# Performance work log

Hardware: AMD Instinct MI355X
Metric: run time of the kernel (lower is better)

The kernel has to match this reference:

```python
import jax, jax.numpy as jnp
import numpy as np

B, D, T, H, E = 4, 1024, 2048, 16, 64  # batch, dim, seq_len, n_heads, hidden_dim (H*E == D)


def setup_inputs() -> dict:
    key = jax.random.key(0)
    ks = jax.random.split(key, 6)
    x = jax.random.normal(ks[0], (B, D, T), dtype=jnp.float32)            # (b, e, t) layout
    Wp = jax.random.normal(ks[1], (H, E, D), dtype=jnp.float32) / np.sqrt(D)  # per-head proj weights
    bp = jax.random.normal(ks[2], (H, E), dtype=jnp.float32) * 0.01
    tw = jax.random.normal(ks[3], (H, T), dtype=jnp.float32) / np.sqrt(T)  # per-head Toeplitz kernel, tw[h,0]=diagonal
    Wo = jax.random.normal(ks[4], (D, D), dtype=jnp.float32) / np.sqrt(D)
    bo = jax.random.normal(ks[5], (D,), dtype=jnp.float32) * 0.01
    return {"x": x, "Wp": Wp, "bp": bp, "tw": tw, "Wo": Wo, "bo": bo}


def reference(x, Wp, bp, tw, Wo, bo):
    # x: (b, dim, t) -> (b, t, dim)
    xt = jnp.transpose(x, (0, 2, 1))
    # per-head projections: (b, h, e, t)
    proj = jnp.einsum('btd,hed->bhet', xt, Wp) + bp[None, :, :, None]
    # build per-head causal lower-triangular Toeplitz matrices: Tm[h, t, s] = tw[h, t-s] if s <= t else 0
    idx = jnp.arange(T)[:, None] - jnp.arange(T)[None, :]  # (t, s)
    Tm = jnp.where(idx >= 0, tw[:, jnp.clip(idx, 0)], 0.0)  # (h, t, s)
    # causal Toeplitz mixing along time per head
    mixed = jnp.einsum('hts,bhes->bhet', Tm, proj)          # (b, h, e, t)
    # concat heads on feature dim: (b, t, h*e) == (b, t, dim)
    cat = jnp.transpose(mixed, (0, 3, 1, 2)).reshape(B, T, H * E)
    out = cat @ Wo.T + bo                                   # out_proj: Linear(dim, dim)
    return jnp.transpose(out, (0, 2, 1))                    # back to (b, e, t)
```

## Files before the change

kernel.cpp:

```cpp
#include <hip/hip_runtime.h>
#include <cstdint>

#define NB 4
#define ND 1024
#define NT 2048
#define NH 16
#define NE 64
#define GLEN 2240
#define CAP 2312

typedef __bf16 bf16x8 __attribute__((ext_vector_type(8)));
typedef float f32x4 __attribute__((ext_vector_type(4)));
typedef unsigned short us8 __attribute__((ext_vector_type(8)));
typedef unsigned short us4 __attribute__((ext_vector_type(4)));

__device__ __forceinline__ unsigned short f2bf(float f) {
  unsigned u = __builtin_bit_cast(unsigned, f);
  return (unsigned short)((u + 0x7fffu + ((u >> 16) & 1u)) >> 16);
}

__device__ __forceinline__ void gload16(const void* g, void* l) {
  __builtin_amdgcn_global_load_lds(
      (const __attribute__((address_space(1))) void*)(uintptr_t)g,
      (__attribute__((address_space(3))) void*)(uintptr_t)l, 16, 0, 0);
}

__global__ __launch_bounds__(256) void prep_transpose(const float* __restrict__ x,
                                                      unsigned short* __restrict__ xT,
                                                      const float* __restrict__ Wp,
                                                      const float* __restrict__ Wo,
                                                      const float* __restrict__ tw,
                                                      unsigned short* __restrict__ WpB,
                                                      unsigned short* __restrict__ WoB,
                                                      unsigned short* __restrict__ Gr8) {
  __shared__ float tile[64][65];
  if (blockIdx.x >= 32) {
    int bid = (blockIdx.x - 32) + 8 * (blockIdx.y + 16 * blockIdx.z);
    int idx = bid * 256 + threadIdx.x;
    const int stride = 512 * 256;
    const int n4 = ND * ND / 4;
    for (int i = idx; i < n4; i += stride) {
      float4 v = ((const float4*)Wp)[i];
      us4 o = {f2bf(v.x), f2bf(v.y), f2bf(v.z), f2bf(v.w)};
      ((us4*)WpB)[i] = o;
    }
    for (int i = idx; i < n4; i += stride) {
      float4 v = ((const float4*)Wo)[i];
      us4 o = {f2bf(v.x), f2bf(v.y), f2bf(v.z), f2bf(v.w)};
      ((us4*)WoB)[i] = o;
    }
    for (int i = idx; i < NH * 8 * GLEN; i += stride) {
      int h = i / (8 * GLEN);
      int rem = i - h * 8 * GLEN;
      int r = rem / GLEN;
      int c = rem - r * GLEN;
      int src = c + r;
      Gr8[i] = (src <= NT - 1) ? f2bf(tw[h * NT + (NT - 1) - src]) : (unsigned short)0;
    }
    return;
  }
  const int c = threadIdx.x & 15, r = threadIdx.x >> 4;
  const int t0 = blockIdx.x * 64, d0 = blockIdx.y * 64, b = blockIdx.z;
  const float* xb = x + (long)b * ND * NT;
#pragma unroll
  for (int k = 0; k < 4; ++k) {
    float4 v = *(const float4*)&xb[(long)(d0 + r + 16 * k) * NT + t0 + 4 * c];
    tile[r + 16 * k][4 * c + 0] = v.x;
    tile[r + 16 * k][4 * c + 1] = v.y;
    tile[r + 16 * k][4 * c + 2] = v.z;
    tile[r + 16 * k][4 * c + 3] = v.w;
  }
  __syncthreads();
  unsigned short* xTb = xT + (long)b * NT * ND;
#pragma unroll
  for (int k = 0; k < 4; ++k) {
    int t = r + 16 * k;
    us4 o = {f2bf(tile[4 * c + 0][t]), f2bf(tile[4 * c + 1][t]), f2bf(tile[4 * c + 2][t]),
             f2bf(tile[4 * c + 3][t])};
    *(us4*)&xTb[(long)(t0 + t) * ND + d0 + 4 * c] = o;
  }
}

template <bool OUT_BF16>
__global__ __launch_bounds__(256, 2) void gemm_bt(const unsigned short* __restrict__ A,
                                                  const unsigned short* __restrict__ Bt,
                                                  const float* __restrict__ bias,
                                                  void* __restrict__ Cb, long strideB,
                                                  long strideC) {
  const int N = 2048, K = 1024;
  __shared__ __align__(16) unsigned short As[2][128 * 64];
  __shared__ __align__(16) unsigned short Bs[2][128 * 64];
  const int tid = threadIdx.x;
  const int lane = tid & 63;
  const int wid = tid >> 6;
  const int wm = (wid & 1) * 64, wn = (wid >> 1) * 64;
  const int m0 = blockIdx.y * 128, n0 = blockIdx.x * 128;
  const unsigned short* Bb = Bt + (long)blockIdx.z * strideB;
  const int mlo = lane & 15, q = lane >> 4, m7 = mlo & 7;

  const unsigned short* aP[4];
  const unsigned short* bP[4];
  int dstc[4];
#pragma unroll
  for (int p = 0; p < 4; ++p) {
    int chunk = p * 256 + tid;
    int row = chunk >> 3, blk = chunk & 7;
    int sc = (blk ^ (row & 7)) * 8;
    aP[p] = A + (long)(m0 + row) * K + sc;
    bP[p] = Bb + (long)(n0 + row) * K + sc;
    dstc[p] = chunk * 8;
  }

  auto stage = [&](int buf, int t) {
#pragma unroll
    for (int p = 0; p < 4; ++p) {
      gload16(aP[p] + t * 64, &As[buf][dstc[p]]);
      gload16(bP[p] + t * 64, &Bs[buf][dstc[p]]);
    }
  };

  f32x4 acc[4][4] = {};
  stage(0, 0);

#pragma unroll
  for (int t = 0; t < 16; ++t) {
    const int buf = t & 1;
    asm volatile("s_waitcnt lgkmcnt(0)" ::: "memory");
    __builtin_amdgcn_s_barrier();
    if (t < 15) stage(buf ^ 1, t + 1);
    if (t < 15)
      asm volatile("s_waitcnt vmcnt(8)" ::: "memory");
    else
      asm volatile("s_waitcnt vmcnt(0)" ::: "memory");
    __builtin_amdgcn_s_barrier();
#pragma unroll
    for (int ks = 0; ks < 2; ++ks) {
      bf16x8 av[4], bv[4];
      const int xb8 = ((4 * ks + q) ^ m7) * 8;
#pragma unroll
      for (int i = 0; i < 4; ++i) {
        av[i] = __builtin_bit_cast(bf16x8, *(const us8*)&As[buf][(wm + i * 16 + mlo) * 64 + xb8]);
        bv[i] = __builtin_bit_cast(bf16x8, *(const us8*)&Bs[buf][(wn + i * 16 + mlo) * 64 + xb8]);
      }
      __builtin_amdgcn_s_setprio(1);
#pragma unroll
      for (int i = 0; i < 4; ++i)
#pragma unroll
        for (int j = 0; j < 4; ++j)
          acc[i][j] = __builtin_amdgcn_mfma_f32_16x16x32_bf16(av[i], bv[j], acc[i][j], 0, 0, 0);
      __builtin_amdgcn_s_setprio(0);
    }
  }

#pragma unroll
  for (int i = 0; i < 4; ++i)
#pragma unroll
    for (int j = 0; j < 4; ++j)
#pragma unroll
      for (int r = 0; r < 4; ++r) {
        int gr = m0 + wm + i * 16 + q * 4 + r;
        int gc = n0 + wn + j * 16 + mlo;
        float v = acc[i][j][r] + bias[gr];
        if (OUT_BF16)
          ((unsigned short*)Cb)[(long)blockIdx.z * strideC + (long)gr * N + gc] = f2bf(v);
        else
          ((float*)Cb)[(long)blockIdx.z * strideC + (long)gr * N + gc] = v;
      }
}

__global__ __launch_bounds__(256, 2) void toeplitz(const unsigned short* __restrict__ proj,
                                                   const unsigned short* __restrict__ Gr8,
                                                   unsigned short* __restrict__ mixedT) {
  __shared__ __align__(16) unsigned short Ls[8 * CAP];
  __shared__ __align__(16) unsigned short Bs[4][2][64 * 32];
  const int tid = threadIdx.x, lane = tid & 63, w = tid >> 6;
  const int j = blockIdx.y, h = blockIdx.x, bz = blockIdx.z;
  const int mlo = lane & 15, q = lane >> 4;
  const int wt = (w >> 1) * 64, we = (w & 1) * 32;
  const int t0L = (15 - j) * 128, t0S = j * 128;

  const int delta = (NT - 128) - t0L;
  const int MUSE = t0L + 256;
#pragma unroll 1
  for (int r = 0; r < 8; ++r) {
    int rr = (r + delta) & 7;
    int off8 = r + delta - rr;
    const unsigned short* src = Gr8 + (long)(h * 8 + rr) * GLEN + off8;
    unsigned short* dst = &Ls[r * CAP];
    for (int mc = tid; mc * 8 < MUSE; mc += 256) gload16(src + mc * 8, dst + mc * 8);
  }

  const int rA = (7 - mlo) & 7;
  const int eRow = tid >> 2;
  const int kCol = (((tid & 3) ^ ((tid >> 3) & 3))) * 8;
  const unsigned short* bsrc = proj + ((long)bz * ND + h * 64 + eRow) * NT + kCol;

  const int nc0 = 2 * (16 - j);
  const int NCT = 34;
  const unsigned short* lA0 = &Ls[rA * CAP + (127 - wt - mlo - rA) + q * 8];
  const unsigned short* lA1 = lA0 + (t0L - t0S);
  const int bswz = (q ^ (((we + mlo) >> 1) & 3)) * 8;

  auto stage = [&](int g) {
    int c = (g < nc0) ? g : g - nc0;
    gload16(bsrc + c * 64, &Bs[g & 3][0][tid * 8]);
    gload16(bsrc + c * 64 + 32, &Bs[g & 3][1][tid * 8]);
  };

  stage(0);
  stage(1);
  stage(2);

  f32x4 acc[4][2];
  bf16x8 ap0 = {}, ap1 = {};
  const unsigned short* lA = lA0;

  auto sub = [&](int bf, int hh, int s) {
    bf16x8 a0 = __builtin_bit_cast(bf16x8, *(const us8*)(lA + s));
    bf16x8 a1 = __builtin_bit_cast(bf16x8, *(const us8*)(lA + s - 16));
    bf16x8 b0 = __builtin_bit_cast(bf16x8, *(const us8*)&Bs[bf][hh][(we + mlo) * 32 + bswz]);
    bf16x8 b1 = __builtin_bit_cast(bf16x8, *(const us8*)&Bs[bf][hh][(we + 16 + mlo) * 32 + bswz]);
    acc[0][0] = __builtin_amdgcn_mfma_f32_16x16x32_bf16(a0, b0, acc[0][0], 0, 0, 0);
    acc[0][1] = __builtin_amdgcn_mfma_f32_16x16x32_bf16(a0, b1, acc[0][1], 0, 0, 0);
    acc[1][0] = __builtin_amdgcn_mfma_f32_16x16x32_bf16(a1, b0, acc[1][0], 0, 0, 0);
    acc[1][1] = __builtin_amdgcn_mfma_f32_16x16x32_bf16(a1, b1, acc[1][1], 0, 0, 0);
    acc[2][0] = __builtin_amdgcn_mfma_f32_16x16x32_bf16(ap0, b0, acc[2][0], 0, 0, 0);
    acc[2][1] = __builtin_amdgcn_mfma_f32_16x16x32_bf16(ap0, b1, acc[2][1], 0, 0, 0);
    acc[3][0] = __builtin_amdgcn_mfma_f32_16x16x32_bf16(ap1, b0, acc[3][0], 0, 0, 0);
    acc[3][1] = __builtin_amdgcn_mfma_f32_16x16x32_bf16(ap1, b1, acc[3][1], 0, 0, 0);
    ap0 = a0;
    ap1 = a1;
  };

#pragma unroll 1
  for (int g = 0; g < NCT; ++g) {
    if (g + 2 < NCT)
      asm volatile("s_waitcnt vmcnt(4) lgkmcnt(0)" ::: "memory");
    else if (g + 1 < NCT)
      asm volatile("s_waitcnt vmcnt(2) lgkmcnt(0)" ::: "memory");
    else
      asm volatile("s_waitcnt vmcnt(0) lgkmcnt(0)" ::: "memory");
    __builtin_amdgcn_s_barrier();
    if (g + 3 < NCT) stage(g + 3);

    const int pass = (g >= nc0) ? 1 : 0;
    const int c = pass ? g - nc0 : g;
    if (c == 0) {
      lA = pass ? lA1 : lA0;
      ap0 = __builtin_bit_cast(bf16x8, *(const us8*)(lA - 32));
      ap1 = __builtin_bit_cast(bf16x8, *(const us8*)(lA - 48));
#pragma unroll
      for (int i = 0; i < 4; ++i)
#pragma unroll
        for (int jj = 0; jj < 2; ++jj) acc[i][jj] = f32x4{0.f, 0.f, 0.f, 0.f};
    }
    const int buf = g & 3;
    const int s0 = c * 64;
    __builtin_amdgcn_s_setprio(1);
    sub(buf, 0, s0);
    sub(buf, 1, s0 + 32);
    __builtin_amdgcn_s_setprio(0);

    if ((!pass && g == nc0 - 1) || g == NCT - 1) {
      const int t0p = pass ? t0S : t0L;
#pragma unroll
      for (int i = 0; i < 4; ++i)
#pragma unroll
        for (int jj = 0; jj < 2; ++jj)
#pragma unroll
          for (int rr = 0; rr < 4; ++rr) {
            int t = t0p + wt + i * 16 + q * 4 + rr;
            int e = we + jj * 16 + mlo;
            mixedT[((long)bz * NT + t) * ND + h * 64 + e] = f2bf(acc[i][jj][rr]);
          }
    }
  }
}

extern "C" void kernel_launch(void* const* d_in, const int* in_sizes, int n_in, void* d_out,
                              int out_size, void* d_ws, size_t ws_size, hipStream_t stream) {
  const float* x = (const float*)d_in[0];
  const float* Wp = (const float*)d_in[1];
  const float* bp = (const float*)d_in[2];
  const float* tw = (const float*)d_in[3];
  const float* Wo = (const float*)d_in[4];
  const float* bo = (const float*)d_in[5];
  float* out = (float*)d_out;

  char* ws = (char*)d_ws;
  unsigned short* xT = (unsigned short*)(ws);
  unsigned short* proj = (unsigned short*)(ws + (16ull << 20));
  unsigned short* WpB = (unsigned short*)(ws + (32ull << 20));
  unsigned short* WoB = (unsigned short*)(ws + (34ull << 20));
  unsigned short* Gr8 = (unsigned short*)(ws + (36ull << 20));

  prep_transpose<<<dim3(40, 16, NB), 256, 0, stream>>>(x, xT, Wp, Wo, tw, WpB, WoB, Gr8);
  gemm_bt<true><<<dim3(16, 8, NB), 256, 0, stream>>>(WpB, xT, bp, proj, (long)NT * ND,
                                                     (long)ND * NT);
  toeplitz<<<dim3(NH, 8, NB), 256, 0, stream>>>(proj, Gr8, xT);
  gemm_bt<false><<<dim3(16, 8, NB), 256, 0, stream>>>(WoB, xT, bo, out, (long)NT * ND,
                                                      (long)ND * NT);
}
```

Before: 159.0 us.

## Enlarge Toeplitz time tile to 256 rows per block with deeper A-register shift

```diff
diff --git a/kernel.cpp b/kernel.cpp
--- a/kernel.cpp
+++ b/kernel.cpp
@@ -6,8 +6,9 @@
 #define NT 2048
 #define NH 16
 #define NE 64
-#define GLEN 2240
+#define GLEN 2304
 #define CAP 2312
+#define TTILE 256
 
 typedef __bf16 bf16x8 __attribute__((ext_vector_type(8)));
 typedef float f32x4 __attribute__((ext_vector_type(4)));
@@ -168,7 +169,7 @@
       }
 }
 
-__global__ __launch_bounds__(256, 2) void toeplitz(const unsigned short* __restrict__ proj,
+__global__ __launch_bounds__(256, 1) void toeplitz(const unsigned short* __restrict__ proj,
                                                    const unsigned short* __restrict__ Gr8,
                                                    unsigned short* __restrict__ mixedT) {
   __shared__ __align__(16) unsigned short Ls[8 * CAP];
@@ -176,11 +177,11 @@
   const int tid = threadIdx.x, lane = tid & 63, w = tid >> 6;
   const int j = blockIdx.y, h = blockIdx.x, bz = blockIdx.z;
   const int mlo = lane & 15, q = lane >> 4;
-  const int wt = (w >> 1) * 64, we = (w & 1) * 32;
-  const int t0L = (15 - j) * 128, t0S = j * 128;
-
-  const int delta = (NT - 128) - t0L;
-  const int MUSE = t0L + 256;
+  const int wt = (w >> 1) * 128, we = (w & 1) * 32;
+  const int t0L = (7 - j) * TTILE, t0S = j * TTILE;
+
+  const int delta = (NT - TTILE) - t0L;
+  const int MUSE = t0L + 2 * TTILE;
 #pragma unroll 1
   for (int r = 0; r < 8; ++r) {
     int rr = (r + delta) & 7;
@@ -195,9 +196,9 @@
   const int kCol = (((tid & 3) ^ ((tid >> 3) & 3))) * 8;
   const unsigned short* bsrc = proj + ((long)bz * ND + h * 64 + eRow) * NT + kCol;
 
-  const int nc0 = 2 * (16 - j);
-  const int NCT = 34;
-  const unsigned short* lA0 = &Ls[rA * CAP + (127 - wt - mlo - rA) + q * 8];
+  const int nc0 = 4 * (8 - j);
+  const int NCT = 36;
+  const unsigned short* lA0 = &Ls[rA * CAP + (255 - wt - mlo - rA) + q * 8];
   const unsigned short* lA1 = lA0 + (t0L - t0S);
   const int bswz = (q ^ (((we + mlo) >> 1) & 3)) * 8;
 
@@ -211,8 +212,8 @@
   stage(1);
   stage(2);
 
-  f32x4 acc[4][2];
-  bf16x8 ap0 = {}, ap1 = {};
+  f32x4 acc[8][2];
+  bf16x8 aq0 = {}, aq1 = {}, aq2 = {}, aq3 = {}, aq4 = {}, aq5 = {};
   const unsigned short* lA = lA0;
 
   auto sub = [&](int bf, int hh, int s) {
@@ -224,12 +225,24 @@
     acc[0][1] = __builtin_amdgcn_mfma_f32_16x16x32_bf16(a0, b1, acc[0][1], 0, 0, 0);
     acc[1][0] = __builtin_amdgcn_mfma_f32_16x16x32_bf16(a1, b0, acc[1][0], 0, 0, 0);
     acc[1][1] = __builtin_amdgcn_mfma_f32_16x16x32_bf16(a1, b1, acc[1][1], 0, 0, 0);
-    acc[2][0] = __builtin_amdgcn_mfma_f32_16x16x32_bf16(ap0, b0, acc[2][0], 0, 0, 0);
-    acc[2][1] = __builtin_amdgcn_mfma_f32_16x16x32_bf16(ap0, b1, acc[2][1], 0, 0, 0);
-    acc[3][0] = __builtin_amdgcn_mfma_f32_16x16x32_bf16(ap1, b0, acc[3][0], 0, 0, 0);
-    acc[3][1] = __builtin_amdgcn_mfma_f32_16x16x32_bf16(ap1, b1, acc[3][1], 0, 0, 0);
-    ap0 = a0;
-    ap1 = a1;
+    acc[2][0] = __builtin_amdgcn_mfma_f32_16x16x32_bf16(aq0, b0, acc[2][0], 0, 0, 0);
+    acc[2][1] = __builtin_amdgcn_mfma_f32_16x16x32_bf16(aq0, b1, acc[2][1], 0, 0, 0);
+    acc[3][0] = __builtin_amdgcn_mfma_f32_16x16x32_bf16(aq1, b0, acc[3][0], 0, 0, 0);
+    acc[3][1] = __builtin_amdgcn_mfma_f32_16x16x32_bf16(aq1, b1, acc[3][1], 0, 0, 0);
+    acc[4][0] = __builtin_amdgcn_mfma_f32_16x16x32_bf16(aq2, b0, acc[4][0], 0, 0, 0);
+    acc[4][1] = __builtin_amdgcn_mfma_f32_16x16x32_bf16(aq2, b1, acc[4][1], 0, 0, 0);
+    acc[5][0] = __builtin_amdgcn_mfma_f32_16x16x32_bf16(aq3, b0, acc[5][0], 0, 0, 0);
+    acc[5][1] = __builtin_amdgcn_mfma_f32_16x16x32_bf16(aq3, b1, acc[5][1], 0, 0, 0);
+    acc[6][0] = __builtin_amdgcn_mfma_f32_16x16x32_bf16(aq4, b0, acc[6][0], 0, 0, 0);
+    acc[6][1] = __builtin_amdgcn_mfma_f32_16x16x32_bf16(aq4, b1, acc[6][1], 0, 0, 0);
+    acc[7][0] = __builtin_amdgcn_mfma_f32_16x16x32_bf16(aq5, b0, acc[7][0], 0, 0, 0);
+    acc[7][1] = __builtin_amdgcn_mfma_f32_16x16x32_bf16(aq5, b1, acc[7][1], 0, 0, 0);
+    aq5 = aq3;
+    aq4 = aq2;
+    aq3 = aq1;
+    aq2 = aq0;
+    aq1 = a1;
+    aq0 = a0;
   };
 
 #pragma unroll 1
@@ -247,10 +260,14 @@
     const int c = pass ? g - nc0 : g;
     if (c == 0) {
       lA = pass ? lA1 : lA0;
-      ap0 = __builtin_bit_cast(bf16x8, *(const us8*)(lA - 32));
-      ap1 = __builtin_bit_cast(bf16x8, *(const us8*)(lA - 48));
-#pragma unroll
-      for (int i = 0; i < 4; ++i)
+      aq0 = __builtin_bit_cast(bf16x8, *(const us8*)(lA - 32));
+      aq1 = __builtin_bit_cast(bf16x8, *(const us8*)(lA - 48));
+      aq2 = __builtin_bit_cast(bf16x8, *(const us8*)(lA - 64));
+      aq3 = __builtin_bit_cast(bf16x8, *(const us8*)(lA - 80));
+      aq4 = __builtin_bit_cast(bf16x8, *(const us8*)(lA - 96));
+      aq5 = __builtin_bit_cast(bf16x8, *(const us8*)(lA - 112));
+#pragma unroll
+      for (int i = 0; i < 8; ++i)
 #pragma unroll
         for (int jj = 0; jj < 2; ++jj) acc[i][jj] = f32x4{0.f, 0.f, 0.f, 0.f};
     }
@@ -264,7 +281,7 @@
     if ((!pass && g == nc0 - 1) || g == NCT - 1) {
       const int t0p = pass ? t0S : t0L;
 #pragma unroll
-      for (int i = 0; i < 4; ++i)
+      for (int i = 0; i < 8; ++i)
 #pragma unroll
         for (int jj = 0; jj < 2; ++jj)
 #pragma unroll
@@ -297,7 +314,7 @@
   prep_transpose<<<dim3(40, 16, NB), 256, 0, stream>>>(x, xT, Wp, Wo, tw, WpB, WoB, Gr8);
   gemm_bt<true><<<dim3(16, 8, NB), 256, 0, stream>>>(WpB, xT, bp, proj, (long)NT * ND,
                                                      (long)ND * NT);
-  toeplitz<<<dim3(NH, 8, NB), 256, 0, stream>>>(proj, Gr8, xT);
+  toeplitz<<<dim3(NH, 4, NB), 256, 0, stream>>>(proj, Gr8, xT);
   gemm_bt<false><<<dim3(16, 8, NB), 256, 0, stream>>>(WoB, xT, bo, out, (long)NT * ND,
                                                       (long)ND * NT);
 }
```

Result: slower. 168.1 us (+5.7%).
